# Performance work log

Measured on AMD Instinct MI355X. Metric: run time of the kernel, lower is better.

The kernel has to match this reference:

```python
import jax, jax.numpy as jnp
import numpy as np
from jax import lax
import math

SCALES = (128.0, 256.0, 512.0)
ASPECT_RATIOS = (0.5, 1.0, 2.0)
NMS_THR = 0.7
PRENMS_TOPK = 2000   # rpn_train_prenms_topk (module is in training mode at __init__)
POST_TOPK = 300      # rpn_train_topk
MIN_SIZE = 16.0      # rpn_min_size
BBOX_CLAMP = math.log(1000.0 / 16.0)


def conv2d(x, w, b, pad):
    y = lax.conv_general_dilated(x, w, (1, 1), pad,
                                 dimension_numbers=('NCHW', 'OIHW', 'NCHW'))
    return y + b[None, :, None, None]


def generate_anchors(img_h, img_w, grid_h, grid_w, dtype=jnp.float32):
    # Mirrors RegionProposalNetwork.generate_anchors
    stride_h = img_h // grid_h
    stride_w = img_w // grid_w
    scales = jnp.asarray(SCALES, dtype)
    ratios = jnp.asarray(ASPECT_RATIOS, dtype)
    h = jnp.sqrt(ratios)
    w = 1.0 / h
    ws = (w[:, None] * scales[None, :]).reshape(-1)   # (K,)
    hs = (h[:, None] * scales[None, :]).reshape(-1)
    base = jnp.round(jnp.stack([-ws, -hs, ws, hs], axis=1) / 2.0)  # (K,4)
    sx = jnp.arange(grid_w, dtype=dtype) * stride_w
    sy = jnp.arange(grid_h, dtype=dtype) * stride_h
    syy, sxx = jnp.meshgrid(sy, sx, indexing='ij')
    sxx = sxx.reshape(-1); syy = syy.reshape(-1)
    shifts = jnp.stack([sxx, syy, sxx, syy], axis=1)               # (HW,4)
    anchors = (shifts[:, None, :] + base[None, :, :]).reshape(-1, 4)  # (HW*K,4)
    return anchors


def decode(deltas, anchors):
    wa = anchors[:, 2] - anchors[:, 0]
    ha = anchors[:, 3] - anchors[:, 1]
    cxa = anchors[:, 0] + 0.5 * wa
    cya = anchors[:, 1] + 0.5 * ha
    dx, dy = deltas[..., 0], deltas[..., 1]
    dw = jnp.minimum(deltas[..., 2], BBOX_CLAMP)
    dh = jnp.minimum(deltas[..., 3], BBOX_CLAMP)
    cx = dx * wa + cxa
    cy = dy * ha + cya
    w = jnp.exp(dw) * wa
    h = jnp.exp(dh) * ha
    return jnp.stack([cx - 0.5 * w, cy - 0.5 * h, cx + 0.5 * w, cy + 0.5 * h], axis=-1)


def pairwise_iou(a, b):
    area_a = (a[:, 2] - a[:, 0]) * (a[:, 3] - a[:, 1])
    area_b = (b[:, 2] - b[:, 0]) * (b[:, 3] - b[:, 1])
    lt = jnp.maximum(a[:, None, :2], b[None, :, :2])
    rb = jnp.minimum(a[:, None, 2:], b[None, :, 2:])
    wh = jnp.clip(rb - lt, 0.0)
    inter = wh[..., 0] * wh[..., 1]
    return inter / (area_a[:, None] + area_b[None, :] - inter)


def nms_keep(boxes, init_suppressed):
    # boxes are already sorted by descending score; O(N^2) matrix NMS.
    iou = lax.stop_gradient(pairwise_iou(boxes, boxes))
    n = boxes.shape[0]
    idxs = jnp.arange(n)
    def body(i, st):
        keep, sup = st
        valid = jnp.logical_not(sup[i])
        keep = keep.at[i].set(valid)
        sup = sup | (valid & (iou[i] > NMS_THR) & (idxs > i))
        return keep, sup
    keep, _ = lax.fori_loop(0, n, body,
                            (jnp.zeros(n, dtype=bool), init_suppressed))
    return keep


def filter_one(proposals, scores, img_h, img_w):
    # pre-NMS top-k
    sc, idx = lax.top_k(scores, PRENMS_TOPK)
    boxes = proposals[idx]
    # clip to image
    x1 = jnp.clip(boxes[:, 0], 0.0, img_w)
    y1 = jnp.clip(boxes[:, 1], 0.0, img_h)
    x2 = jnp.clip(boxes[:, 2], 0.0, img_w)
    y2 = jnp.clip(boxes[:, 3], 0.0, img_h)
    boxes = jnp.stack([x1, y1, x2, y2], axis=1)
    # min-size filter (masked, fixed shape)
    small = ((x2 - x1) < MIN_SIZE) | ((y2 - y1) < MIN_SIZE)
    sc = jnp.where(small, -jnp.inf, sc)
    # NMS then post-NMS top-k
    keep = nms_keep(boxes, small)
    post = jnp.where(keep, sc, -jnp.inf)
    fs, fi = lax.top_k(post, POST_TOPK)
    return boxes[fi], fs


def setup_inputs() -> dict:
    key = jax.random.key(0)
    ks = jax.random.split(key, 8)
    B, C, H, W, IMG, K = 4, 512, 64, 64, 1024, 9
    image = jax.random.normal(ks[0], (B, 3, IMG, IMG), jnp.float32)
    feature_map = jax.random.normal(ks[1], (B, C, H, W), jnp.float32)
    # init: normal(std=0.01) weights, zero bias
    w_conv = 0.01 * jax.random.normal(ks[2], (C, C, 3, 3), jnp.float32)
    b_conv = jnp.zeros((C,), jnp.float32)
    w_cls = 0.01 * jax.random.normal(ks[3], (K, C, 1, 1), jnp.float32)
    b_cls = jnp.zeros((K,), jnp.float32)
    w_box = 0.01 * jax.random.normal(ks[4], (4 * K, C, 1, 1), jnp.float32)
    b_box = jnp.zeros((4 * K,), jnp.float32)
    return {"image": image, "feature_map": feature_map,
            "w_conv": w_conv, "b_conv": b_conv,
            "w_cls": w_cls, "b_cls": b_cls,
            "w_box": w_box, "b_box": b_box}


def reference(image, feature_map, w_conv, b_conv, w_cls, b_cls, w_box, b_box):
    B, _, img_h, img_w = image.shape
    _, _, gh, gw = feature_map.shape
    feat = jax.nn.relu(conv2d(feature_map, w_conv, b_conv, 'SAME'))
    cls = conv2d(feat, w_cls, b_cls, 'VALID')   # (B, K, H, W)
    box = conv2d(feat, w_box, b_box, 'VALID')   # (B, 4K, H, W)
    scores = jax.nn.sigmoid(cls.transpose(0, 2, 3, 1).reshape(B, -1))   # (B, N)
    deltas = box.transpose(0, 2, 3, 1).reshape(B, -1, 4)                # (B, N, 4)
    anchors = generate_anchors(img_h, img_w, gh, gw)                    # (N, 4)
    proposals = decode(deltas, anchors)                                 # (B, N, 4)
    props, sc = jax.vmap(lambda p, s: filter_one(p, s, float(img_h), float(img_w)))(proposals, scores)
    return props, sc   # (B, POST_TOPK, 4), (B, POST_TOPK)
```

## Files before the change

kernel.cpp:

```cpp
#include <hip/hip_runtime.h>
#include <math.h>

typedef unsigned long long U64;
typedef _Float16 half8 __attribute__((ext_vector_type(8)));
typedef float f32x16 __attribute__((ext_vector_type(16)));

__device__ const float g_bw[9] = {91.f, 181.f, 362.f, 64.f, 128.f, 256.f, 45.f, 91.f, 181.f};
__device__ const float g_bh[9] = {45.f, 91.f, 181.f, 64.f, 128.f, 256.f, 91.f, 181.f, 362.f};

__device__ inline f32x16 zero16() {
    f32x16 z;
#pragma unroll
    for (int i = 0; i < 16; ++i) z[i] = 0.f;
    return z;
}

#define GLOAD16(G, L)                                                  \
    __builtin_amdgcn_global_load_lds(                                  \
        (const __attribute__((address_space(1))) void*)(G),            \
        (__attribute__((address_space(3))) void*)(L), 16, 0, 0)

__global__ __launch_bounds__(256) void k_prep_fm(const float* __restrict__ fm,
                                                 _Float16* __restrict__ fpi) {
    int bid = blockIdx.x, b = blockIdx.y;
    int t = threadIdx.x;
    if (bid >= 512) {
        int ci = bid - 512;
        int hp, wp;
        if (ci < 66)       { hp = 0;  wp = ci; }
        else if (ci < 132) { hp = 65; wp = ci - 66; }
        else { int k = ci - 132; hp = 1 + (k & 63); wp = (k < 64) ? 0 : 65; }
        uint2 z; z.x = 0u; z.y = 0u;
        *(uint2*)(fpi + ((size_t)(b * 66 + hp) * 66 + wp) * 1024 + t * 4) = z;
        return;
    }
    __shared__ float tile[64][65];
    int cg = bid & 7, h = bid >> 3;
    int cl = t >> 2, w0 = (t & 3) * 16;
    const float* src = fm + (((size_t)(b * 512 + cg * 64 + cl) * 64 + h) * 64 + w0);
#pragma unroll
    for (int l = 0; l < 4; ++l) {
        float4 v = *(const float4*)(src + l * 4);
        tile[cl][w0 + l * 4 + 0] = v.x; tile[cl][w0 + l * 4 + 1] = v.y;
        tile[cl][w0 + l * 4 + 2] = v.z; tile[cl][w0 + l * 4 + 3] = v.w;
    }
    __syncthreads();
    int w = t & 63, pth = t >> 6;
    int chunkrel = pth >> 1, half = pth & 1;
    _Float16* dst = fpi + ((size_t)((b * 66 + h + 1) * 66) + (w + 1)) * 1024 +
                    (cg * 2 + chunkrel) * 64 + half * 32;
#pragma unroll
    for (int g8 = 0; g8 < 4; ++g8) {
        half8 v;
#pragma unroll
        for (int i = 0; i < 8; ++i) {
            float x = tile[chunkrel * 32 + g8 * 8 + i][w];
            _Float16 hi = (_Float16)x;
            v[i] = half ? (_Float16)((x - (float)hi) * 2048.0f) : hi;
        }
        *(half8*)(dst + g8 * 8) = v;
    }
}

__global__ __launch_bounds__(256) void k_prep_w(const float* __restrict__ w_conv,
                                                _Float16* __restrict__ wki) {
    __shared__ float wb[4608];
    int o = blockIdx.x, t = threadIdx.x;
    for (int e = t; e < 4608; e += 256) wb[e] = w_conv[(size_t)o * 4608 + e];
    __syncthreads();
    for (int e = t; e < 9216; e += 256) {
        int s = e & 63, chunk = e >> 6;
        int tap = chunk >> 4, cgi = chunk & 15;
        int c = cgi * 32 + (s & 31);
        float x = wb[c * 9 + tap];
        _Float16 hi = (_Float16)x;
        wki[(size_t)o * 9216 + e] = (s < 32) ? hi : (_Float16)((x - (float)hi) * 2048.0f);
    }
}

__global__ __launch_bounds__(256, 2) void k_conv_mfma(
    const _Float16* __restrict__ fpi, const _Float16* __restrict__ wki,
    const float* __restrict__ bconv, float* __restrict__ feat) {
    __shared__ _Float16 As[2][128][64];
    __shared__ _Float16 Bs[2][128][64];
    const int t = threadIdx.x;
    const int lane = t & 63, wv = t >> 6;
    const int wm = wv >> 1, wn = wv & 1;
    int flat = (int)blockIdx.x + 128 * (int)blockIdx.y;
    int fid = (flat & 7) * 64 + (flat >> 3);
    const int p0 = (fid >> 2) * 128, o0 = (fid & 3) * 128;

    const char* baseA[4];
    const char* baseB[4];
#pragma unroll
    for (int q = 0; q < 4; ++q) {
        int row = wv * 32 + q * 8 + (lane >> 3);
        int qs = (lane & 7) ^ (row & 7);
        int P = p0 + row;
        int bb = P >> 12, hh = (P >> 6) & 63, ww = P & 63;
        baseA[q] = (const char*)fpi + ((size_t)((bb * 66 + hh) * 66 + ww)) * 2048 + qs * 16;
        baseB[q] = (const char*)wki + (size_t)(o0 + row) * 18432 + qs * 16;
    }

    f32x16 acc0[2][2], acc1[2][2];
#pragma unroll
    for (int mi = 0; mi < 2; ++mi)
#pragma unroll
        for (int ni = 0; ni < 2; ++ni) { acc0[mi][ni] = zero16(); acc1[mi][ni] = zero16(); }

    auto issue = [&](int it2, int buf) {
        int tap = it2 >> 4;
        int ry = (tap * 11) >> 5, rx = tap - ry * 3;
        int ka = (ry * 66 + rx) * 2048 + (it2 & 15) * 128;
        int kb = it2 * 128;
#pragma unroll
        for (int q = 0; q < 4; ++q) {
            GLOAD16(baseA[q] + ka, &As[buf][wv * 32 + q * 8][0]);
            GLOAD16(baseB[q] + kb, &Bs[buf][wv * 32 + q * 8][0]);
        }
    };

    issue(0, 0);
    issue(1, 1);

#define LOADA(mi_)                                                              \
    {                                                                           \
        int rA = wm * 64 + (mi_) * 32 + (lane & 31);                            \
        int xa = (rA & 7) << 4, ba = rA * 128;                                  \
        af[mi_][0][0] = *(const half8*)(ab + ba + ((0 + lg) ^ xa));             \
        af[mi_][0][1] = *(const half8*)(ab + ba + ((32 + lg) ^ xa));            \
        af[mi_][1][0] = *(const half8*)(ab + ba + ((64 + lg) ^ xa));            \
        af[mi_][1][1] = *(const half8*)(ab + ba + ((96 + lg) ^ xa));            \
    }
#define LOADB(ni_)                                                              \
    {                                                                           \
        int rB = wn * 64 + (ni_) * 32 + (lane & 31);                            \
        int xb = (rB & 7) << 4, bb0 = rB * 128;                                 \
        bf[ni_][0][0] = *(const half8*)(bb2 + bb0 + ((0 + lg) ^ xb));           \
        bf[ni_][0][1] = *(const half8*)(bb2 + bb0 + ((32 + lg) ^ xb));          \
        bf[ni_][1][0] = *(const half8*)(bb2 + bb0 + ((64 + lg) ^ xb));          \
        bf[ni_][1][1] = *(const half8*)(bb2 + bb0 + ((96 + lg) ^ xb));          \
    }
#define QUAD(mi_, ni_)                                                                                     \
    acc0[mi_][ni_] = __builtin_amdgcn_mfma_f32_32x32x16_f16(af[mi_][0][0], bf[ni_][0][0], acc0[mi_][ni_], 0, 0, 0); \
    acc0[mi_][ni_] = __builtin_amdgcn_mfma_f32_32x32x16_f16(af[mi_][0][1], bf[ni_][0][1], acc0[mi_][ni_], 0, 0, 0); \
    acc1[mi_][ni_] = __builtin_amdgcn_mfma_f32_32x32x16_f16(af[mi_][0][0], bf[ni_][1][0], acc1[mi_][ni_], 0, 0, 0); \
    acc1[mi_][ni_] = __builtin_amdgcn_mfma_f32_32x32x16_f16(af[mi_][0][1], bf[ni_][1][1], acc1[mi_][ni_], 0, 0, 0); \
    acc1[mi_][ni_] = __builtin_amdgcn_mfma_f32_32x32x16_f16(af[mi_][1][0], bf[ni_][0][0], acc1[mi_][ni_], 0, 0, 0); \
    acc1[mi_][ni_] = __builtin_amdgcn_mfma_f32_32x32x16_f16(af[mi_][1][1], bf[ni_][0][1], acc1[mi_][ni_], 0, 0, 0);

    for (int it = 0; it < 144; ++it) {
        int cur = it & 1;
        if (it < 143) { asm volatile("s_waitcnt vmcnt(8)" ::: "memory"); }
        else          { asm volatile("s_waitcnt vmcnt(0)" ::: "memory"); }
        __builtin_amdgcn_s_barrier();
        __builtin_amdgcn_sched_barrier(0);

        const char* ab = (const char*)As + cur * 16384;
        const char* bb2 = (const char*)Bs + cur * 16384;
        const int lg = (lane >> 5) * 16;
        half8 af[2][2][2], bf[2][2][2];

        LOADA(0) LOADB(0) LOADA(1)
        __builtin_amdgcn_s_setprio(1);
        QUAD(0, 0)
        __builtin_amdgcn_s_setprio(0);
        LOADB(1)
        __builtin_amdgcn_s_setprio(1);
        QUAD(1, 0) QUAD(0, 1) QUAD(1, 1)
        __builtin_amdgcn_s_setprio(0);

        __builtin_amdgcn_sched_group_barrier(0x100, 12, 0);
        __builtin_amdgcn_sched_group_barrier(0x008, 6, 0);
        __builtin_amdgcn_sched_group_barrier(0x100, 4, 0);
        __builtin_amdgcn_sched_group_barrier(0x008, 18, 0);

        __builtin_amdgcn_sched_barrier(0);
        __builtin_amdgcn_s_barrier();
        __builtin_amdgcn_sched_barrier(0);
        if (it < 142) issue(it + 2, cur);
    }

#pragma unroll
    for (int mi = 0; mi < 2; ++mi)
#pragma unroll
        for (int ni = 0; ni < 2; ++ni) {
            int col = o0 + wn * 64 + ni * 32 + (lane & 31);
            float bv = bconv[col];
            int rbase = p0 + wm * 64 + mi * 32 + 4 * (lane >> 5);
#pragma unroll
            for (int q = 0; q < 16; ++q) {
                int row = rbase + (q & 3) + 8 * (q >> 2);
                float v = acc0[mi][ni][q] + acc1[mi][ni][q] * 4.8828125e-4f + bv;
                feat[(size_t)row * 512 + col] = fmaxf(v, 0.f);
            }
        }
}

__global__ __launch_bounds__(256) void k_heads(const float* __restrict__ feat,
                                               const float* __restrict__ w_cls,
                                               const float* __restrict__ b_cls,
                                               const float* __restrict__ w_box,
                                               const float* __restrict__ b_box,
                                               U64* __restrict__ keys,
                                               float4* __restrict__ proposals) {
    __shared__ float red[3][64][45];
    int t = threadIdx.x;
    int px = t & 63, cq = t >> 6;
    int p = blockIdx.x * 64 + px;
    const float* fr = feat + (size_t)p * 512 + cq * 128;
    float acc[45];
#pragma unroll
    for (int o = 0; o < 45; ++o) acc[o] = 0.f;
    for (int c = 0; c < 128; c += 4) {
        float4 f = *(const float4*)(fr + c);
#pragma unroll
        for (int o = 0; o < 45; ++o) {
            const float* wr = ((o < 9) ? (w_cls + o * 512) : (w_box + (o - 9) * 512)) + cq * 128 + c;
            acc[o] += f.x * wr[0] + f.y * wr[1] + f.z * wr[2] + f.w * wr[3];
        }
    }
    if (cq > 0) {
#pragma unroll
        for (int o = 0; o < 45; ++o) red[cq - 1][px][o] = acc[o];
    }
    __syncthreads();
    if (cq == 0) {
#pragma unroll
        for (int o = 0; o < 45; ++o) acc[o] += red[0][px][o] + red[1][px][o] + red[2][px][o];
        int b = p >> 12, pixloc = p & 4095;
        int h = pixloc >> 6, w = pixloc & 63;
        int ibase = b * 36864 + pixloc * 9;
#pragma unroll
        for (int a = 0; a < 9; ++a) {
            float logit = acc[a] + b_cls[a];
            float s = 1.f / (1.f + expf(-logit));
            keys[ibase + a] = (((U64)(__float_as_uint(s) ^ 0x80000000u)) << 32) |
                              (unsigned)(~(unsigned)(pixloc * 9 + a));
            float dx = acc[9 + a * 4 + 0] + b_box[a * 4 + 0];
            float dy = acc[9 + a * 4 + 1] + b_box[a * 4 + 1];
            float dw = fminf(acc[9 + a * 4 + 2] + b_box[a * 4 + 2], 4.135166556742356f);
            float dh = fminf(acc[9 + a * 4 + 3] + b_box[a * 4 + 3], 4.135166556742356f);
            float wa = 2.f * g_bw[a], ha = 2.f * g_bh[a];
            float cx = dx * wa + (float)(w * 16);
            float cy = dy * ha + (float)(h * 16);
            float pw = expf(dw) * wa;
            float ph = expf(dh) * ha;
            proposals[ibase + a] =
                make_float4(cx - 0.5f * pw, cy - 0.5f * ph, cx + 0.5f * pw, cy + 0.5f * ph);
        }
    }
}

__device__ inline void cmp_stage(U64* s, int j, int k, int tid) {
    for (int p = tid; p < 1024; p += 256) {
        int il = ((p & ~(j - 1)) << 1) | (p & (j - 1));
        int ip = il | j;
        U64 a = s[il], c = s[ip];
        bool desc = ((il & k) == 0);
        bool sw = desc ? (a < c) : (a > c);
        if (sw) { s[il] = c; s[ip] = a; }
    }
}

__global__ __launch_bounds__(256) void k_sort_chunk(const U64* __restrict__ keys,
                                                    U64* __restrict__ run) {
    __shared__ U64 s[2048];
    int b = blockIdx.x / 18, ch = blockIdx.x % 18;
    int tid = threadIdx.x;
    const U64* src = keys + (size_t)b * 36864 + ch * 2048;
    for (int e = tid; e < 2048; e += 256) s[e] = src[e];
    __syncthreads();
    for (int k = 2; k <= 2048; k <<= 1)
        for (int j = k >> 1; j >= 1; j >>= 1) {
            cmp_stage(s, j, k, tid);
            __syncthreads();
        }
    U64* dst = run + ((size_t)b * 18 + ch) * 2048;
    for (int e = tid; e < 2048; e += 256) dst[e] = s[e];
}

__global__ __launch_bounds__(256) void k_merge4(const U64* __restrict__ in,
                                                U64* __restrict__ out, int nc) {
    __shared__ U64 s[4096];
    int g = blockIdx.x, b = blockIdx.y;
    int tid = threadIdx.x;
    int r0 = g * 4;
    int n = nc - r0; if (n > 4) n = 4;
    const U64* base = in + (size_t)b * 18 * 2048;
    U64* O = out + ((size_t)b * 18 + g) * 2048;
    for (int e = tid; e < 2048; e += 256) s[e] = base[(size_t)r0 * 2048 + e];
    for (int m = 1; m < n; ++m) {
        for (int e = tid; e < 2048; e += 256) s[4095 - e] = base[(size_t)(r0 + m) * 2048 + e];
        __syncthreads();
        for (int e = tid; e < 2048; e += 256) {
            U64 a = s[e], c = s[e + 2048];
            s[e] = (a >= c) ? a : c;
        }
        __syncthreads();
        for (int j = 1024; j >= 1; j >>= 1) {
            for (int p = tid; p < 1024; p += 256) {
                int il = ((p & ~(j - 1)) << 1) | (p & (j - 1));
                int ip = il | j;
                U64 a = s[il], c = s[ip];
                if (a < c) { s[il] = c; s[ip] = a; }
            }
            __syncthreads();
        }
    }
    for (int e = tid; e < 2048; e += 256) O[e] = s[e];
}

__global__ __launch_bounds__(256) void k_topk_gather(const U64* __restrict__ runf,
                                                     const float4* __restrict__ proposals,
                                                     float4* __restrict__ tb_boxes,
                                                     float* __restrict__ tb_scores) {
    int g = blockIdx.x * 256 + threadIdx.x;
    if (g >= 8000) return;
    int b = g / 2000, r = g - b * 2000;
    U64 key = runf[(size_t)b * 18 * 2048 + r];
    unsigned n = ~((unsigned)key);
    float s = __uint_as_float(((unsigned)(key >> 32)) ^ 0x80000000u);
    float4 p = proposals[b * 36864 + (int)n];
    float x1 = fminf(fmaxf(p.x, 0.f), 1024.f);
    float y1 = fminf(fmaxf(p.y, 0.f), 1024.f);
    float x2 = fminf(fmaxf(p.z, 0.f), 1024.f);
    float y2 = fminf(fmaxf(p.w, 0.f), 1024.f);
    bool small_ = ((x2 - x1) < 16.f) || ((y2 - y1) < 16.f);
    tb_boxes[g] = make_float4(x1, y1, x2, y2);
    tb_scores[g] = small_ ? -INFINITY : s;
}

__global__ __launch_bounds__(64) void k_nms_mask(const float4* __restrict__ tb_boxes,
                                                 U64* __restrict__ mask) {
    int jt = blockIdx.x, it = blockIdx.y, b = blockIdx.z;
    int tid = threadIdx.x;
    __shared__ float4 jb[64];
    int j0 = jt * 64;
    {
        int j = j0 + tid;
        jb[tid] = (j < 2000) ? tb_boxes[b * 2000 + j] : make_float4(0.f, 0.f, 0.f, 0.f);
    }
    __syncthreads();
    int i = it * 64 + tid;
    if (i >= 2000) return;
    float4 bi = tb_boxes[b * 2000 + i];
    float ai = (bi.z - bi.x) * (bi.w - bi.y);
    U64 bits = 0;
#pragma unroll 4
    for (int jj = 0; jj < 64; ++jj) {
        int j = j0 + jj;
        float4 bj = jb[jj];
        float aj = (bj.z - bj.x) * (bj.w - bj.y);
        float ltx = fmaxf(bi.x, bj.x), lty = fmaxf(bi.y, bj.y);
        float rbx = fminf(bi.z, bj.z), rby = fminf(bi.w, bj.w);
        float ww = fmaxf(rbx - ltx, 0.f), hh2 = fmaxf(rby - lty, 0.f);
        float inter = ww * hh2;
        float iou = inter / (ai + aj - inter);
        if ((j > i) && (j < 2000) && (iou > 0.7f)) bits |= (1ull << jj);
    }
    mask[((size_t)b * 2000 + i) * 32 + jt] = bits;
}

__global__ __launch_bounds__(64) void k_nms_scan(const float4* __restrict__ tb_boxes,
                                                 const float* __restrict__ tb_scores,
                                                 const U64* __restrict__ mask,
                                                 float* __restrict__ out) {
    int b = blockIdx.x;
    int lane = threadIdx.x;
    __shared__ unsigned short keeplist[2000];
    __shared__ unsigned char keepflag[2000];
    __shared__ unsigned short fillq[304];

    U64 remv = 0;
    if (lane < 32) {
        for (int jj = 0; jj < 64; ++jj) {
            int j = (lane << 6) | jj;
            if (j < 2000 && tb_scores[b * 2000 + j] == -INFINITY) remv |= (1ull << jj);
        }
    }
    const U64* mb = mask + (size_t)b * 2000 * 32;

    U64 cva[32], cvb[32];
    int nkeep = 0;

    auto loadchunk = [&](U64 (&cv)[32], int ch) {
#pragma unroll
        for (int q = 0; q < 32; ++q) {
            int row = ch * 64 + q * 2 + (lane >> 5), wd = lane & 31;
            cv[q] = (row < 2000) ? mb[(size_t)row * 32 + wd] : 0ull;
        }
    };
    auto process = [&](U64 (&cv)[32], int ch) {
        int base = ch * 64;
        int iend = (2000 - base < 64) ? (2000 - base) : 64;
        U64 w_all = __shfl(remv, ch);
#pragma unroll
        for (int ii = 0; ii < 64; ++ii) {
            if (ii < iend) {
                bool sup = (w_all >> ii) & 1ull;
                int i = base + ii;
                if (!sup) {
                    if (lane == 0) keeplist[nkeep] = (unsigned short)i;
                    U64 mrow = __shfl(cv[ii >> 1], ((ii & 1) << 5) | (lane & 31));
                    if (lane < 32) remv |= mrow;
                    w_all |= __shfl(cv[ii >> 1], ((ii & 1) << 5) | ch);
                    nkeep++;
                }
                if (lane == 0) keepflag[i] = sup ? (unsigned char)0 : (unsigned char)1;
            }
        }
    };

    loadchunk(cva, 0);
    for (int ch2 = 0; ch2 < 32; ch2 += 2) {
        loadchunk(cvb, ch2 + 1);
        process(cva, ch2);
        if (ch2 + 2 < 32) loadchunk(cva, ch2 + 2);
        process(cvb, ch2 + 1);
    }
    __syncthreads();

    if (lane == 0) {
        int need = 300 - nkeep, c = 0;
        for (int i = 0; i < 2000 && c < need; ++i)
            if (!keepflag[i]) fillq[c++] = (unsigned short)i;
    }
    __syncthreads();
    for (int r = lane; r < 300; r += 64) {
        int src; float sc;
        if (r < nkeep) { src = keeplist[r]; sc = tb_scores[b * 2000 + src]; }
        else           { src = fillq[r - nkeep]; sc = -INFINITY; }
        float4 bx = tb_boxes[b * 2000 + src];
        int ob = (b * 300 + r) * 4;
        out[ob + 0] = bx.x; out[ob + 1] = bx.y; out[ob + 2] = bx.z; out[ob + 3] = bx.w;
        out[4800 + b * 300 + r] = sc;
    }
}

extern "C" void kernel_launch(void* const* d_in, const int* in_sizes, int n_in,
                              void* d_out, int out_size, void* d_ws, size_t ws_size,
                              hipStream_t stream) {
    (void)in_sizes; (void)n_in; (void)out_size; (void)ws_size;
    const float* feature_map = (const float*)d_in[1];
    const float* w_conv = (const float*)d_in[2];
    const float* b_conv = (const float*)d_in[3];
    const float* w_cls  = (const float*)d_in[4];
    const float* b_cls  = (const float*)d_in[5];
    const float* w_box  = (const float*)d_in[6];
    const float* b_box  = (const float*)d_in[7];
    float* out = (float*)d_out;

    char* ws = (char*)d_ws;
    size_t off = 0;
    auto alloc = [&](size_t bytes) {
        void* p = ws + off;
        off = (off + bytes + 255) & ~(size_t)255;
        return p;
    };
    const size_t fpi_elems = 4ull * 66 * 66 * 1024;
    _Float16* fpi = (_Float16*)alloc(fpi_elems * 2);
    _Float16* wki = (_Float16*)alloc(512ull * 9216 * 2);
    float*  feat      = (float*) alloc(16384ull * 512 * 4);
    float4* proposals = (float4*)alloc(4ull * 36864 * 16);
    U64*    keys      = (U64*)   alloc(4ull * 36864 * 8);
    U64*    run0      = (U64*)   alloc(4ull * 18 * 2048 * 8);
    U64*    run1      = (U64*)   alloc(4ull * 18 * 2048 * 8);
    float4* tb_boxes  = (float4*)alloc(8000ull * 16);
    float*  tb_scores = (float*) alloc(8000ull * 4);
    U64*    nmsmask   = (U64*)   alloc(8000ull * 32 * 8);

    k_prep_fm<<<dim3(772, 4), 256, 0, stream>>>(feature_map, fpi);
    k_prep_w<<<512, 256, 0, stream>>>(w_conv, wki);
    k_conv_mfma<<<dim3(128, 4), 256, 0, stream>>>(fpi, wki, b_conv, feat);
    k_heads<<<256, 256, 0, stream>>>(feat, w_cls, b_cls, w_box, b_box, keys, proposals);

    k_sort_chunk<<<72, 256, 0, stream>>>(keys, run0);
    k_merge4<<<dim3(5, 4), 256, 0, stream>>>(run0, run1, 18);
    k_merge4<<<dim3(2, 4), 256, 0, stream>>>(run1, run0, 5);
    k_merge4<<<dim3(1, 4), 256, 0, stream>>>(run0, run1, 2);

    k_topk_gather<<<32, 256, 0, stream>>>(run1, proposals, tb_boxes, tb_scores);
    k_nms_mask<<<dim3(32, 32, 4), 64, 0, stream>>>(tb_boxes, nmsmask);
    k_nms_scan<<<4, 64, 0, stream>>>(tb_boxes, tb_scores, nmsmask, out);
}
```

Before: 760.3 us.

## Fuse prep kernels, software-pipeline conv LDS reads, merge sort stages with gather

Combines the feature-map and weight preparation into a single launch. Restructures the MFMA conv main loop so the LDS fragment loads for the next tile are issued during the second half of the current tile's MFMAs, and global prefetch moves earlier. Replaces three hierarchical merge launches plus the top-k gather with one kernel per batch that merges all 18 runs sequentially and gathers the boxes. This cuts launch count and exposed LDS latency, but the single-block-per-batch merge has far less parallelism.

```diff
diff --git a/kernel.cpp b/kernel.cpp
--- a/kernel.cpp
+++ b/kernel.cpp
@@ -20,10 +20,27 @@
         (const __attribute__((address_space(1))) void*)(G),            \
         (__attribute__((address_space(3))) void*)(L), 16, 0, 0)
 
-__global__ __launch_bounds__(256) void k_prep_fm(const float* __restrict__ fm,
-                                                 _Float16* __restrict__ fpi) {
+__global__ __launch_bounds__(256) void k_prep(const float* __restrict__ fm,
+                                              const float* __restrict__ w_conv,
+                                              _Float16* __restrict__ fpi,
+                                              _Float16* __restrict__ wki) {
+    __shared__ float smem[4608];
     int bid = blockIdx.x, b = blockIdx.y;
     int t = threadIdx.x;
+    if (bid >= 772) {
+        int o = (bid - 772) + b * 128;
+        for (int e = t; e < 4608; e += 256) smem[e] = w_conv[(size_t)o * 4608 + e];
+        __syncthreads();
+        for (int e = t; e < 9216; e += 256) {
+            int s = e & 63, chunk = e >> 6;
+            int tap = chunk >> 4, cgi = chunk & 15;
+            int c = cgi * 32 + (s & 31);
+            float x = smem[c * 9 + tap];
+            _Float16 hi = (_Float16)x;
+            wki[(size_t)o * 9216 + e] = (s < 32) ? hi : (_Float16)((x - (float)hi) * 2048.0f);
+        }
+        return;
+    }
     if (bid >= 512) {
         int ci = bid - 512;
         int hp, wp;
@@ -34,7 +51,7 @@
         *(uint2*)(fpi + ((size_t)(b * 66 + hp) * 66 + wp) * 1024 + t * 4) = z;
         return;
     }
-    __shared__ float tile[64][65];
+    float (*tile)[65] = (float(*)[65])smem;
     int cg = bid & 7, h = bid >> 3;
     int cl = t >> 2, w0 = (t & 3) * 16;
     const float* src = fm + (((size_t)(b * 512 + cg * 64 + cl) * 64 + h) * 64 + w0);
@@ -59,22 +76,6 @@
             v[i] = half ? (_Float16)((x - (float)hi) * 2048.0f) : hi;
         }
         *(half8*)(dst + g8 * 8) = v;
-    }
-}
-
-__global__ __launch_bounds__(256) void k_prep_w(const float* __restrict__ w_conv,
-                                                _Float16* __restrict__ wki) {
-    __shared__ float wb[4608];
-    int o = blockIdx.x, t = threadIdx.x;
-    for (int e = t; e < 4608; e += 256) wb[e] = w_conv[(size_t)o * 4608 + e];
-    __syncthreads();
-    for (int e = t; e < 9216; e += 256) {
-        int s = e & 63, chunk = e >> 6;
-        int tap = chunk >> 4, cgi = chunk & 15;
-        int c = cgi * 32 + (s & 31);
-        float x = wb[c * 9 + tap];
-        _Float16 hi = (_Float16)x;
-        wki[(size_t)o * 9216 + e] = (s < 32) ? hi : (_Float16)((x - (float)hi) * 2048.0f);
     }
 }
 
@@ -120,26 +121,26 @@
         }
     };
 
-    issue(0, 0);
-    issue(1, 1);
-
-#define LOADA(mi_)                                                              \
+    const int lg = (lane >> 5) * 16;
+    half8 af[2][2][2], bf[2][2][2];
+
+#define LOADA(mi_, P_)                                                          \
     {                                                                           \
         int rA = wm * 64 + (mi_) * 32 + (lane & 31);                            \
         int xa = (rA & 7) << 4, ba = rA * 128;                                  \
-        af[mi_][0][0] = *(const half8*)(ab + ba + ((0 + lg) ^ xa));             \
-        af[mi_][0][1] = *(const half8*)(ab + ba + ((32 + lg) ^ xa));            \
-        af[mi_][1][0] = *(const half8*)(ab + ba + ((64 + lg) ^ xa));            \
-        af[mi_][1][1] = *(const half8*)(ab + ba + ((96 + lg) ^ xa));            \
-    }
-#define LOADB(ni_)                                                              \
+        af[mi_][0][0] = *(const half8*)((P_) + ba + ((0 + lg) ^ xa));           \
+        af[mi_][0][1] = *(const half8*)((P_) + ba + ((32 + lg) ^ xa));          \
+        af[mi_][1][0] = *(const half8*)((P_) + ba + ((64 + lg) ^ xa));          \
+        af[mi_][1][1] = *(const half8*)((P_) + ba + ((96 + lg) ^ xa));          \
+    }
+#define LOADB(ni_, P_)                                                          \
     {                                                                           \
         int rB = wn * 64 + (ni_) * 32 + (lane & 31);                            \
         int xb = (rB & 7) << 4, bb0 = rB * 128;                                 \
-        bf[ni_][0][0] = *(const half8*)(bb2 + bb0 + ((0 + lg) ^ xb));           \
-        bf[ni_][0][1] = *(const half8*)(bb2 + bb0 + ((32 + lg) ^ xb));          \
-        bf[ni_][1][0] = *(const half8*)(bb2 + bb0 + ((64 + lg) ^ xb));          \
-        bf[ni_][1][1] = *(const half8*)(bb2 + bb0 + ((96 + lg) ^ xb));          \
+        bf[ni_][0][0] = *(const half8*)((P_) + bb0 + ((0 + lg) ^ xb));          \
+        bf[ni_][0][1] = *(const half8*)((P_) + bb0 + ((32 + lg) ^ xb));         \
+        bf[ni_][1][0] = *(const half8*)((P_) + bb0 + ((64 + lg) ^ xb));         \
+        bf[ni_][1][1] = *(const half8*)((P_) + bb0 + ((96 + lg) ^ xb));         \
     }
 #define QUAD(mi_, ni_)                                                                                     \
     acc0[mi_][ni_] = __builtin_amdgcn_mfma_f32_32x32x16_f16(af[mi_][0][0], bf[ni_][0][0], acc0[mi_][ni_], 0, 0, 0); \
@@ -149,36 +150,49 @@
     acc1[mi_][ni_] = __builtin_amdgcn_mfma_f32_32x32x16_f16(af[mi_][1][0], bf[ni_][0][0], acc1[mi_][ni_], 0, 0, 0); \
     acc1[mi_][ni_] = __builtin_amdgcn_mfma_f32_32x32x16_f16(af[mi_][1][1], bf[ni_][0][1], acc1[mi_][ni_], 0, 0, 0);
 
+    issue(0, 0);
+    issue(1, 1);
+    asm volatile("s_waitcnt vmcnt(8)" ::: "memory");
+    __builtin_amdgcn_s_barrier();
+    __builtin_amdgcn_sched_barrier(0);
+    {
+        const char* ab = (const char*)As;
+        const char* bb2 = (const char*)Bs;
+        LOADA(0, ab) LOADA(1, ab) LOADB(0, bb2) LOADB(1, bb2)
+    }
+
     for (int it = 0; it < 144; ++it) {
         int cur = it & 1;
-        if (it < 143) { asm volatile("s_waitcnt vmcnt(8)" ::: "memory"); }
-        else          { asm volatile("s_waitcnt vmcnt(0)" ::: "memory"); }
+        asm volatile("s_waitcnt lgkmcnt(0)" ::: "memory");
+        __builtin_amdgcn_sched_barrier(0);
         __builtin_amdgcn_s_barrier();
         __builtin_amdgcn_sched_barrier(0);
-
-        const char* ab = (const char*)As + cur * 16384;
-        const char* bb2 = (const char*)Bs + cur * 16384;
-        const int lg = (lane >> 5) * 16;
-        half8 af[2][2][2], bf[2][2][2];
-
-        LOADA(0) LOADB(0) LOADA(1)
+        if (it <= 141) issue(it + 2, cur);
+        __builtin_amdgcn_sched_barrier(0);
         __builtin_amdgcn_s_setprio(1);
-        QUAD(0, 0)
+        QUAD(0, 0) QUAD(1, 0)
         __builtin_amdgcn_s_setprio(0);
-        LOADB(1)
-        __builtin_amdgcn_s_setprio(1);
-        QUAD(1, 0) QUAD(0, 1) QUAD(1, 1)
-        __builtin_amdgcn_s_setprio(0);
-
-        __builtin_amdgcn_sched_group_barrier(0x100, 12, 0);
-        __builtin_amdgcn_sched_group_barrier(0x008, 6, 0);
-        __builtin_amdgcn_sched_group_barrier(0x100, 4, 0);
-        __builtin_amdgcn_sched_group_barrier(0x008, 18, 0);
-
+        __builtin_amdgcn_sched_barrier(0);
+        if (it <= 141)      { asm volatile("s_waitcnt vmcnt(8)" ::: "memory"); }
+        else if (it == 142) { asm volatile("s_waitcnt vmcnt(0)" ::: "memory"); }
         __builtin_amdgcn_sched_barrier(0);
         __builtin_amdgcn_s_barrier();
         __builtin_amdgcn_sched_barrier(0);
-        if (it < 142) issue(it + 2, cur);
+        if (it <= 142) {
+            const char* ab = (const char*)As + (cur ^ 1) * 16384;
+            const char* bb2 = (const char*)Bs + (cur ^ 1) * 16384;
+            LOADB(0, bb2)
+            __builtin_amdgcn_s_setprio(1);
+            QUAD(0, 1)
+            __builtin_amdgcn_s_setprio(0);
+            LOADA(0, ab)
+            __builtin_amdgcn_s_setprio(1);
+            QUAD(1, 1)
+            __builtin_amdgcn_s_setprio(0);
+            LOADA(1, ab) LOADB(1, bb2)
+        } else {
+            QUAD(0, 1) QUAD(1, 1)
+        }
     }
 
 #pragma unroll
@@ -280,18 +294,16 @@
     for (int e = tid; e < 2048; e += 256) dst[e] = s[e];
 }
 
-__global__ __launch_bounds__(256) void k_merge4(const U64* __restrict__ in,
-                                                U64* __restrict__ out, int nc) {
+__global__ __launch_bounds__(256) void k_merge_all(const U64* __restrict__ run,
+                                                   const float4* __restrict__ proposals,
+                                                   float4* __restrict__ tb_boxes,
+                                                   float* __restrict__ tb_scores) {
     __shared__ U64 s[4096];
-    int g = blockIdx.x, b = blockIdx.y;
-    int tid = threadIdx.x;
-    int r0 = g * 4;
-    int n = nc - r0; if (n > 4) n = 4;
-    const U64* base = in + (size_t)b * 18 * 2048;
-    U64* O = out + ((size_t)b * 18 + g) * 2048;
-    for (int e = tid; e < 2048; e += 256) s[e] = base[(size_t)r0 * 2048 + e];
-    for (int m = 1; m < n; ++m) {
-        for (int e = tid; e < 2048; e += 256) s[4095 - e] = base[(size_t)(r0 + m) * 2048 + e];
+    int b = blockIdx.x, tid = threadIdx.x;
+    const U64* base = run + (size_t)b * 18 * 2048;
+    for (int e = tid; e < 2048; e += 256) s[e] = base[e];
+    for (int m = 1; m < 18; ++m) {
+        for (int e = tid; e < 2048; e += 256) s[4095 - e] = base[(size_t)m * 2048 + e];
         __syncthreads();
         for (int e = tid; e < 2048; e += 256) {
             U64 a = s[e], c = s[e + 2048];
@@ -308,27 +320,19 @@
             __syncthreads();
         }
     }
-    for (int e = tid; e < 2048; e += 256) O[e] = s[e];
-}
-
-__global__ __launch_bounds__(256) void k_topk_gather(const U64* __restrict__ runf,
-                                                     const float4* __restrict__ proposals,
-                                                     float4* __restrict__ tb_boxes,
-                                                     float* __restrict__ tb_scores) {
-    int g = blockIdx.x * 256 + threadIdx.x;
-    if (g >= 8000) return;
-    int b = g / 2000, r = g - b * 2000;
-    U64 key = runf[(size_t)b * 18 * 2048 + r];
-    unsigned n = ~((unsigned)key);
-    float s = __uint_as_float(((unsigned)(key >> 32)) ^ 0x80000000u);
-    float4 p = proposals[b * 36864 + (int)n];
-    float x1 = fminf(fmaxf(p.x, 0.f), 1024.f);
-    float y1 = fminf(fmaxf(p.y, 0.f), 1024.f);
-    float x2 = fminf(fmaxf(p.z, 0.f), 1024.f);
-    float y2 = fminf(fmaxf(p.w, 0.f), 1024.f);
-    bool small_ = ((x2 - x1) < 16.f) || ((y2 - y1) < 16.f);
-    tb_boxes[g] = make_float4(x1, y1, x2, y2);
-    tb_scores[g] = small_ ? -INFINITY : s;
+    for (int r = tid; r < 2000; r += 256) {
+        U64 key = s[r];
+        unsigned n = ~((unsigned)key);
+        float sc = __uint_as_float(((unsigned)(key >> 32)) ^ 0x80000000u);
+        float4 p = proposals[b * 36864 + (int)n];
+        float x1 = fminf(fmaxf(p.x, 0.f), 1024.f);
+        float y1 = fminf(fmaxf(p.y, 0.f), 1024.f);
+        float x2 = fminf(fmaxf(p.z, 0.f), 1024.f);
+        float y2 = fminf(fmaxf(p.w, 0.f), 1024.f);
+        bool small_ = ((x2 - x1) < 16.f) || ((y2 - y1) < 16.f);
+        tb_boxes[b * 2000 + r] = make_float4(x1, y1, x2, y2);
+        tb_scores[b * 2000 + r] = small_ ? -INFINITY : sc;
+    }
 }
 
 __global__ __launch_bounds__(64) void k_nms_mask(const float4* __restrict__ tb_boxes,
@@ -465,22 +469,15 @@
     float4* proposals = (float4*)alloc(4ull * 36864 * 16);
     U64*    keys      = (U64*)   alloc(4ull * 36864 * 8);
     U64*    run0      = (U64*)   alloc(4ull * 18 * 2048 * 8);
-    U64*    run1      = (U64*)   alloc(4ull * 18 * 2048 * 8);
     float4* tb_boxes  = (float4*)alloc(8000ull * 16);
     float*  tb_scores = (float*) alloc(8000ull * 4);
     U64*    nmsmask   = (U64*)   alloc(8000ull * 32 * 8);
 
-    k_prep_fm<<<dim3(772, 4), 256, 0, stream>>>(feature_map, fpi);
-    k_prep_w<<<512, 256, 0, stream>>>(w_conv, wki);
+    k_prep<<<dim3(900, 4), 256, 0, stream>>>(feature_map, w_conv, fpi, wki);
     k_conv_mfma<<<dim3(128, 4), 256, 0, stream>>>(fpi, wki, b_conv, feat);
     k_heads<<<256, 256, 0, stream>>>(feat, w_cls, b_cls, w_box, b_box, keys, proposals);
-
     k_sort_chunk<<<72, 256, 0, stream>>>(keys, run0);
-    k_merge4<<<dim3(5, 4), 256, 0, stream>>>(run0, run1, 18);
-    k_merge4<<<dim3(2, 4), 256, 0, stream>>>(run1, run0, 5);
-    k_merge4<<<dim3(1, 4), 256, 0, stream>>>(run0, run1, 2);
-
-    k_topk_gather<<<32, 256, 0, stream>>>(run1, proposals, tb_boxes, tb_scores);
+    k_merge_all<<<4, 256, 0, stream>>>(run0, proposals, tb_boxes, tb_scores);
     k_nms_mask<<<dim3(32, 32, 4), 64, 0, stream>>>(tb_boxes, nmsmask);
     k_nms_scan<<<4, 64, 0, stream>>>(tb_boxes, tb_scores, nmsmask, out);
 }
```

New measurement: 794.1 us. 1.04x slower.
